# Performance work log

Measured on AMD Instinct MI355X. Metric: run time of the kernel, lower is better.

The kernel has to match this reference:

```python
import jax, jax.numpy as jnp
import numpy as np

N_NODES = 12000
N_EDGES = 384000
F_IN = 128       # num_features
D = 64           # latent_dim (hidden_dim), num_gc_layers = 1
H_DEC = 64       # ceil(F_IN / 2)
BN_EPS = 1e-4


def _gcn_conv(x, W, b, src, dst, n):
    # PyG GCNConv: h = x @ W; add self-loops; sym-normalized scatter-add; + bias
    h = x @ W
    loop = jnp.arange(n)
    s = jnp.concatenate([src, loop])
    d = jnp.concatenate([dst, loop])
    deg = jax.ops.segment_sum(jnp.ones(s.shape[0], dtype=x.dtype), d, num_segments=n)
    dis = jax.lax.rsqrt(deg)  # deg >= 1 thanks to self-loops
    norm = dis[s] * dis[d]    # [E+N]
    out = jax.ops.segment_sum(h[s] * norm[:, None], d, num_segments=n)
    return out + b


def _bn_train(x, gamma, beta):
    # BatchNorm1d, training-mode batch statistics, biased variance, eps=1e-4
    mu = jnp.mean(x, axis=0)
    xc = x - mu
    var = jnp.mean(xc * xc, axis=0)
    return xc * jax.lax.rsqrt(var + BN_EPS) * gamma + beta


def _enc_layer(x, W, b, g, be, src, dst, n):
    # GCNConv -> Sigmoid -> (dropout no-op) -> BatchNorm
    return _bn_train(jax.nn.sigmoid(_gcn_conv(x, W, b, src, dst, n)), g, be)


def setup_inputs() -> dict:
    key = jax.random.key(0)
    ks = jax.random.split(key, 16)
    inp = {
        'x': jax.random.normal(ks[0], (N_NODES, F_IN), dtype=jnp.float32),
        'src': jax.random.randint(ks[1], (N_EDGES,), 0, N_NODES),
        'dst': jax.random.randint(ks[2], (N_EDGES,), 0, N_NODES),
        'batch': jnp.zeros((N_NODES,), dtype=jnp.int32),
        'noise': jax.random.normal(ks[3], (N_NODES, D), dtype=jnp.float32),
        # base_gcn encoder (GCNConv F_IN -> D, BN)
        'W0': jax.random.normal(ks[4], (F_IN, D), dtype=jnp.float32) * 0.08,
        'b0': jnp.zeros((D,), dtype=jnp.float32),
        'g0': jnp.ones((D,), dtype=jnp.float32),
        'be0': jnp.zeros((D,), dtype=jnp.float32),
        # gcn_mean encoder (GCNConv D -> D, BN)
        'Wm': jax.random.normal(ks[5], (D, D), dtype=jnp.float32) * 0.12,
        'bm': jnp.zeros((D,), dtype=jnp.float32),
        'gm': jnp.ones((D,), dtype=jnp.float32),
        'bem': jnp.zeros((D,), dtype=jnp.float32),
        # gcn_logstddev encoder (GCNConv D -> D, BN)
        'Ws': jax.random.normal(ks[6], (D, D), dtype=jnp.float32) * 0.12,
        'bs': jnp.zeros((D,), dtype=jnp.float32),
        'gs': jnp.ones((D,), dtype=jnp.float32),
        'bes': jnp.zeros((D,), dtype=jnp.float32),
        # decoder MLP: Linear(D, H_DEC) -> LeakyReLU -> Linear(H_DEC, F_IN)
        'Dw1': jax.random.normal(ks[7], (D, H_DEC), dtype=jnp.float32) * 0.12,
        'Db1': jnp.zeros((H_DEC,), dtype=jnp.float32),
        'Dw2': jax.random.normal(ks[8], (H_DEC, F_IN), dtype=jnp.float32) * 0.12,
        'Db2': jnp.zeros((F_IN,), dtype=jnp.float32),
    }
    return inp


def reference(x, src, dst, batch, noise,
              W0, b0, g0, be0,
              Wm, bm, gm, bem,
              Ws, bs, gs, bes,
              Dw1, Db1, Dw2, Db2):
    n = x.shape[0]
    hidden = _enc_layer(x, W0, b0, g0, be0, src, dst, n)          # [N, D]
    mean = _enc_layer(hidden, Wm, bm, gm, bem, src, dst, n)       # [N, D]
    logstd = _enc_layer(hidden, Ws, bs, gs, bes, src, dst, n)     # [N, D]
    z = noise * jnp.exp(logstd) + mean                            # reparam trick
    # decoder MLP (LeakyReLU default slope 0.01)
    h = jax.nn.leaky_relu(z @ Dw1 + Db1, negative_slope=0.01)
    reconstructed_x = h @ Dw2 + Db2                               # [N, F_IN]
    A_pred = jax.nn.sigmoid(z @ z.T)                              # [N, N]
    return (reconstructed_x, A_pred)
```

## Files before the change

kernel.cpp:

```cpp
#include <hip/hip_runtime.h>
#include <hip/hip_bf16.h>

#define N_NODES 12000
#define N_EDGES 384000
#define F_INN   128
#define DLAT    64
#define BN_EPS  1e-4f

typedef __attribute__((ext_vector_type(8))) short bf16x8;
typedef __attribute__((ext_vector_type(4))) float f32x4;

__device__ __forceinline__ float sigmoidf(float x) { return 1.0f / (1.0f + __expf(-x)); }

__device__ __forceinline__ unsigned short f2bf_rne(float x) {
    unsigned u = __float_as_uint(x);
    unsigned r = (u + 0x7fffu + ((u >> 16) & 1u)) >> 16;
    return (unsigned short)r;
}
__device__ __forceinline__ float bf2f(unsigned short h) {
    return __uint_as_float((unsigned)h << 16);
}

__global__ void k_init(int* cnt, int* cur, int n) {
    int i = blockIdx.x * blockDim.x + threadIdx.x;
    if (i < n) { cnt[i] = 0; cur[i] = 0; }
}

__global__ void k_count(const int* dst, int* cnt, int e) {
    int i = blockIdx.x * blockDim.x + threadIdx.x;
    if (i < e) atomicAdd(&cnt[dst[i]], 1);
}

__global__ void k_scan(const int* __restrict__ cnt, int* __restrict__ offs,
                       float* __restrict__ dis, int n) {
    __shared__ int wsum[16];
    int tid = threadIdx.x;
    int base = tid * 12;
    int v[12];
    int s = 0;
#pragma unroll
    for (int q = 0; q < 12; q++) {
        int i = base + q;
        v[q] = (i < n) ? cnt[i] : 0;
        s += v[q];
        if (i < n) dis[i] = rsqrtf((float)(v[q] + 1));
    }
    int lane = tid & 63, w = tid >> 6;
    int ps = s;
#pragma unroll
    for (int o = 1; o < 64; o <<= 1) {
        int t2 = __shfl_up(ps, o, 64);
        if (lane >= o) ps += t2;
    }
    if (lane == 63) wsum[w] = ps;
    __syncthreads();
    if (tid == 0) {
        int acc = 0;
        for (int i = 0; i < 16; i++) { int t2 = wsum[i]; wsum[i] = acc; acc += t2; }
    }
    __syncthreads();
    int acc = wsum[w] + ps - s;
#pragma unroll
    for (int q = 0; q < 12; q++) {
        int i = base + q;
        if (i < n) offs[i] = acc;
        acc += v[q];
        if (i == n - 1) offs[n] = acc;
    }
}

__global__ void k_scatter(const int* src, const int* dst, const int* offs, int* cur,
                          int* ssrc, int e) {
    int i = blockIdx.x * blockDim.x + threadIdx.x;
    if (i < e) {
        int d = dst[i];
        int p = atomicAdd(&cur[d], 1);
        ssrc[offs[d] + p] = src[i];
    }
}

__global__ void k_mm(const float* __restrict__ X, int n, int K,
                     const float* __restrict__ Wa, int Ma,
                     const float* __restrict__ Wb, int Mb,
                     float* __restrict__ out) {
    __shared__ float Wl[8192];
    int M = Ma + Mb;
    for (int idx = threadIdx.x; idx < K * M; idx += blockDim.x) {
        int k = idx / M, m = idx % M;
        Wl[idx] = (m < Ma) ? Wa[k * Ma + m] : Wb[k * Mb + (m - Ma)];
    }
    __syncthreads();
    int rpb = blockDim.x / M;
    int r = blockIdx.x * rpb + threadIdx.x / M;
    int m = threadIdx.x % M;
    if (r >= n) return;
    const float* xr = X + (size_t)r * K;
    float acc = 0.f;
    for (int k = 0; k < K; k++) acc += xr[k] * Wl[k * M + m];
    out[(size_t)r * M + m] = acc;
}

__global__ void k_agg(const float* __restrict__ h, const float* __restrict__ dis,
                      const int* __restrict__ offs, const int* __restrict__ ssrc,
                      const float* __restrict__ ba, const float* __restrict__ bb, int Ma,
                      float* __restrict__ out, int dim, int n) {
    int t = blockIdx.x * blockDim.x + threadIdx.x;
    int node = t / dim;
    if (node >= n) return;
    int f = t - node * dim;
    float di = dis[node];
    float acc = h[(size_t)node * dim + f] * di;
    int e0 = offs[node], e1 = offs[node + 1];
    int j = e0;
    for (; j + 3 < e1; j += 4) {
        int s0 = ssrc[j], s1 = ssrc[j + 1], s2 = ssrc[j + 2], s3 = ssrc[j + 3];
        acc += h[(size_t)s0 * dim + f] * dis[s0];
        acc += h[(size_t)s1 * dim + f] * dis[s1];
        acc += h[(size_t)s2 * dim + f] * dis[s2];
        acc += h[(size_t)s3 * dim + f] * dis[s3];
    }
    for (; j < e1; j++) {
        int s = ssrc[j];
        acc += h[(size_t)s * dim + f] * dis[s];
    }
    float bias = (f < Ma) ? ba[f] : bb[f - Ma];
    out[(size_t)node * dim + f] = sigmoidf(acc * di + bias);
}

#define STATS_BLOCKS 64
__global__ void k_stats1(const float* __restrict__ act, int dim, int n,
                         float* __restrict__ part) {
    int rpb = 256 / dim;
    int c = threadIdx.x % dim;
    int rloc = threadIdx.x / dim;
    float s = 0.f, s2 = 0.f;
    for (int r = blockIdx.x * rpb + rloc; r < n; r += STATS_BLOCKS * rpb) {
        float v = act[(size_t)r * dim + c];
        s += v; s2 += v * v;
    }
    __shared__ float sh[512];
    sh[threadIdx.x] = s; sh[256 + threadIdx.x] = s2;
    __syncthreads();
    if (rloc == 0) {
        for (int q = 1; q < rpb; q++) {
            s += sh[q * dim + c];
            s2 += sh[256 + q * dim + c];
        }
        part[(size_t)(blockIdx.x * dim + c) * 2] = s;
        part[(size_t)(blockIdx.x * dim + c) * 2 + 1] = s2;
    }
}

__global__ void k_stats2(const float* __restrict__ part, int dim, int n,
                         float* __restrict__ mu, float* __restrict__ var) {
    int c = threadIdx.x;
    if (c >= dim) return;
    float s = 0.f, s2 = 0.f;
    for (int q = 0; q < STATS_BLOCKS; q++) {
        s += part[(size_t)(q * dim + c) * 2];
        s2 += part[(size_t)(q * dim + c) * 2 + 1];
    }
    float m = s / n;
    mu[c] = m;
    var[c] = s2 / n - m * m;
}

__global__ void k_bnapply(const float* __restrict__ in, float* __restrict__ out,
                          const float* __restrict__ mu, const float* __restrict__ var,
                          const float* __restrict__ g, const float* __restrict__ be,
                          int dim, size_t total) {
    size_t i = (size_t)blockIdx.x * blockDim.x + threadIdx.x;
    if (i >= total) return;
    int f = (int)(i % dim);
    out[i] = (in[i] - mu[f]) * rsqrtf(var[f] + BN_EPS) * g[f] + be[f];
}

__global__ void k_z(const float* __restrict__ act2, const float* __restrict__ noise,
                    const float* __restrict__ mu, const float* __restrict__ var,
                    const float* __restrict__ gm, const float* __restrict__ bem,
                    const float* __restrict__ gs, const float* __restrict__ bes,
                    float* __restrict__ z, unsigned short* __restrict__ zh,
                    unsigned short* __restrict__ zl, int n) {
    int i = blockIdx.x * blockDim.x + threadIdx.x;
    if (i >= 12032 * 64) return;
    int row = i >> 6, j = i & 63;
    if (row >= n) { zh[i] = 0; zl[i] = 0; return; }
    const float* ar = act2 + (size_t)row * 128;
    float m  = (ar[j]      - mu[j])      * rsqrtf(var[j]      + BN_EPS) * gm[j] + bem[j];
    float ls = (ar[j + 64] - mu[j + 64]) * rsqrtf(var[j + 64] + BN_EPS) * gs[j] + bes[j];
    float zv = noise[i] * __expf(ls) + m;
    z[i] = zv;
    unsigned short h = f2bf_rne(zv);
    zh[i] = h;
    zl[i] = f2bf_rne(zv - bf2f(h));
}

__global__ void k_dec(const float* __restrict__ z,
                      const float* __restrict__ W1, const float* __restrict__ B1,
                      const float* __restrict__ W2, const float* __restrict__ B2,
                      float* __restrict__ out, int n) {
    __shared__ float w1[64 * 64];
    __shared__ float w2[64 * 128];
    __shared__ float zl[16 * 64];
    __shared__ float hl[16 * 64];
    int t = threadIdx.x;
    int row0 = blockIdx.x * 16;
    {
        const float4* W14 = (const float4*)W1;
        const float4* W24 = (const float4*)W2;
        for (int i = t; i < 1024; i += 256) ((float4*)w1)[i] = W14[i];
        for (int i = t; i < 2048; i += 256) ((float4*)w2)[i] = W24[i];
        ((float4*)zl)[t] = ((const float4*)(z + (size_t)row0 * 64))[t];
    }
    __syncthreads();
    {
        int hc = t & 63, rg = t >> 6;
        float a0 = B1[hc], a1 = a0, a2 = a0, a3 = a0;
        int rb = rg * 4;
        for (int k = 0; k < 64; k++) {
            float wv = w1[k * 64 + hc];
            a0 += zl[(rb + 0) * 64 + k] * wv;
            a1 += zl[(rb + 1) * 64 + k] * wv;
            a2 += zl[(rb + 2) * 64 + k] * wv;
            a3 += zl[(rb + 3) * 64 + k] * wv;
        }
        hl[(rb + 0) * 64 + hc] = a0 > 0.f ? a0 : 0.01f * a0;
        hl[(rb + 1) * 64 + hc] = a1 > 0.f ? a1 : 0.01f * a1;
        hl[(rb + 2) * 64 + hc] = a2 > 0.f ? a2 : 0.01f * a2;
        hl[(rb + 3) * 64 + hc] = a3 > 0.f ? a3 : 0.01f * a3;
    }
    __syncthreads();
    {
        int oc = t & 127, rg = t >> 7;
        float o[8];
#pragma unroll
        for (int i = 0; i < 8; i++) o[i] = B2[oc];
        int rb = rg * 8;
        for (int k = 0; k < 64; k++) {
            float wv = w2[k * 128 + oc];
#pragma unroll
            for (int i = 0; i < 8; i++) o[i] += hl[(rb + i) * 64 + k] * wv;
        }
#pragma unroll
        for (int i = 0; i < 8; i++)
            out[(size_t)(row0 + rb + i) * 128 + oc] = o[i];
    }
}

#define TN2 94
__global__ __launch_bounds__(256) void k_apred(const unsigned short* __restrict__ zh,
                                               const unsigned short* __restrict__ zl,
                                               float* __restrict__ out, int n) {
    int b = blockIdx.x;
    float ff = (float)(2 * TN2 + 1);
    int bi = (int)((ff - sqrtf(ff * ff - 8.0f * (float)b)) * 0.5f);
    while (bi > 0 && b < bi * TN2 - bi * (bi - 1) / 2) bi--;
    while (b >= (bi + 1) * TN2 - (bi + 1) * bi / 2) bi++;
    int bj = bi + (b - (bi * TN2 - bi * (bi - 1) / 2));
    int i0 = bi * 128, j0 = bj * 128;

    int t = threadIdx.x;
    int wave = t >> 6, lane = t & 63;
    int wr = wave >> 1, wc = wave & 1;
    int lrow = lane & 15;
    int kg   = lane >> 4;

    int arow0 = i0 + wr * 64;
    int brow0 = j0 + wc * 64;

    f32x4 acc[4][4] = {};

#pragma unroll
    for (int kc = 0; kc < 2; kc++) {
        int koff = kc * 32 + kg * 8;
        bf16x8 ah[4], al[4], bh[4], bl[4];
#pragma unroll
        for (int f = 0; f < 4; f++) {
            size_t aoff = (size_t)(arow0 + f * 16 + lrow) * 64 + koff;
            ah[f] = *(const bf16x8*)(zh + aoff);
            al[f] = *(const bf16x8*)(zl + aoff);
            size_t boff = (size_t)(brow0 + f * 16 + lrow) * 64 + koff;
            bh[f] = *(const bf16x8*)(zh + boff);
            bl[f] = *(const bf16x8*)(zl + boff);
        }
#pragma unroll
        for (int fi = 0; fi < 4; fi++)
#pragma unroll
            for (int fj = 0; fj < 4; fj++) {
                acc[fi][fj] = __builtin_amdgcn_mfma_f32_16x16x32_bf16(
                    ah[fi], bh[fj], acc[fi][fj], 0, 0, 0);
                acc[fi][fj] = __builtin_amdgcn_mfma_f32_16x16x32_bf16(
                    ah[fi], bl[fj], acc[fi][fj], 0, 0, 0);
                acc[fi][fj] = __builtin_amdgcn_mfma_f32_16x16x32_bf16(
                    al[fi], bh[fj], acc[fi][fj], 0, 0, 0);
            }
    }

#pragma unroll
    for (int fi = 0; fi < 4; fi++)
#pragma unroll
        for (int fj = 0; fj < 4; fj++)
#pragma unroll
            for (int q = 0; q < 4; q++)
                acc[fi][fj][q] = sigmoidf(acc[fi][fj][q]);

#pragma unroll
    for (int fi = 0; fi < 4; fi++) {
#pragma unroll
        for (int q = 0; q < 4; q++) {
            int r = arow0 + fi * 16 + kg * 4 + q;
            if (r < n) {
#pragma unroll
                for (int fj = 0; fj < 4; fj++) {
                    int c = brow0 + fj * 16 + lrow;
                    if (c < n) out[(size_t)r * n + c] = acc[fi][fj][q];
                }
            }
        }
    }
    if (bi != bj) {
#pragma unroll
        for (int fj = 0; fj < 4; fj++) {
            int c = brow0 + fj * 16 + lrow;
            if (c < n) {
#pragma unroll
                for (int fi = 0; fi < 4; fi++) {
#pragma unroll
                    for (int q = 0; q < 4; q++) {
                        int r = arow0 + fi * 16 + kg * 4 + q;
                        if (r < n) out[(size_t)c * n + r] = acc[fi][fj][q];
                    }
                }
            }
        }
    }
}

extern "C" void kernel_launch(void* const* d_in, const int* in_sizes, int n_in,
                              void* d_out, int out_size, void* d_ws, size_t ws_size,
                              hipStream_t stream) {
    const float* x     = (const float*)d_in[0];
    const int*   src   = (const int*)d_in[1];
    const int*   dst   = (const int*)d_in[2];
    const float* noise = (const float*)d_in[4];
    const float* W0  = (const float*)d_in[5];
    const float* b0  = (const float*)d_in[6];
    const float* g0  = (const float*)d_in[7];
    const float* be0 = (const float*)d_in[8];
    const float* Wm  = (const float*)d_in[9];
    const float* bm  = (const float*)d_in[10];
    const float* gm  = (const float*)d_in[11];
    const float* bem = (const float*)d_in[12];
    const float* Ws  = (const float*)d_in[13];
    const float* bs  = (const float*)d_in[14];
    const float* gs  = (const float*)d_in[15];
    const float* bes = (const float*)d_in[16];
    const float* Dw1 = (const float*)d_in[17];
    const float* Db1 = (const float*)d_in[18];
    const float* Dw2 = (const float*)d_in[19];
    const float* Db2 = (const float*)d_in[20];
    float* out = (float*)d_out;

    const int n = N_NODES, e = N_EDGES;

    int*   cnt  = (int*)d_ws;
    int*   offs = (int*)d_ws + 12032;
    int*   cur  = (int*)d_ws + 24064;
    int*   ssrc = (int*)d_ws + 36096;
    float* dis  = (float*)d_ws + 420096;
    float* mu   = (float*)d_ws + 432128;
    float* var  = (float*)d_ws + 432384;
    float* part = (float*)d_ws + 432640;
    float* bufA = (float*)d_ws + 449024;
    float* bufB = bufA + (size_t)N_NODES * 128;
    float* zbuf = bufB;
    unsigned short* zhbuf = (unsigned short*)((float*)d_ws + 3521024);
    unsigned short* zlbuf = (unsigned short*)((float*)d_ws + 3906048);

    k_init<<<(n + 255) / 256, 256, 0, stream>>>(cnt, cur, n);
    k_count<<<(e + 255) / 256, 256, 0, stream>>>(dst, cnt, e);
    k_scan<<<1, 1024, 0, stream>>>(cnt, offs, dis, n);
    k_scatter<<<(e + 255) / 256, 256, 0, stream>>>(src, dst, offs, cur, ssrc, e);

    k_mm<<<n / 4, 256, 0, stream>>>(x, n, F_INN, W0, DLAT, nullptr, 0, bufA);
    k_agg<<<(n * DLAT) / 256, 256, 0, stream>>>(bufA, dis, offs, ssrc, b0, nullptr, DLAT,
                                                bufB, DLAT, n);
    k_stats1<<<STATS_BLOCKS, 256, 0, stream>>>(bufB, DLAT, n, part);
    k_stats2<<<1, 64, 0, stream>>>(part, DLAT, n, mu, var);
    k_bnapply<<<(n * DLAT) / 256, 256, 0, stream>>>(bufB, bufA, mu, var, g0, be0, DLAT,
                                                    (size_t)n * DLAT);

    k_mm<<<n / 2, 256, 0, stream>>>(bufA, n, DLAT, Wm, DLAT, Ws, DLAT, bufB);
    k_agg<<<(n * 128) / 256, 256, 0, stream>>>(bufB, dis, offs, ssrc, bm, bs, DLAT,
                                               bufA, 128, n);
    k_stats1<<<STATS_BLOCKS, 256, 0, stream>>>(bufA, 128, n, part);
    k_stats2<<<1, 128, 0, stream>>>(part, 128, n, mu, var);

    k_z<<<(12032 * 64) / 256, 256, 0, stream>>>(bufA, noise, mu, var, gm, bem, gs, bes,
                                                zbuf, zhbuf, zlbuf, n);

    k_dec<<<n / 16, 256, 0, stream>>>(zbuf, Dw1, Db1, Dw2, Db2, out, n);

    k_apred<<<TN2 * (TN2 + 1) / 2, 256, 0, stream>>>(zhbuf, zlbuf,
                                                     out + (size_t)n * F_INN, n);
}
```

Before: 1.048 ms.

## Compute full A_pred grid with LDS-staged swizzled tiles instead of symmetric triangle

Replaces the triangular-block launch that wrote each tile and its transpose with a full 2D grid where each block computes only its own 128x128 tile. The z hi/lo tiles are staged into XOR-swizzled shared memory before the MFMA loop, and launch bounds request two blocks per CU. This drops the uncoalesced transposed stores, which dominate the 576 MB output write, at the cost of doubling the MFMA compute and the z reads.

```diff
diff --git a/kernel.cpp b/kernel.cpp
--- a/kernel.cpp
+++ b/kernel.cpp
@@ -248,40 +248,57 @@
 }
 
 #define TN2 94
-__global__ __launch_bounds__(256) void k_apred(const unsigned short* __restrict__ zh,
-                                               const unsigned short* __restrict__ zl,
-                                               float* __restrict__ out, int n) {
-    int b = blockIdx.x;
-    float ff = (float)(2 * TN2 + 1);
-    int bi = (int)((ff - sqrtf(ff * ff - 8.0f * (float)b)) * 0.5f);
-    while (bi > 0 && b < bi * TN2 - bi * (bi - 1) / 2) bi--;
-    while (b >= (bi + 1) * TN2 - (bi + 1) * bi / 2) bi++;
-    int bj = bi + (b - (bi * TN2 - bi * (bi - 1) / 2));
+__global__ __launch_bounds__(256, 2) void k_apred(const unsigned short* __restrict__ zh,
+                                                  const unsigned short* __restrict__ zl,
+                                                  float* __restrict__ out, int n) {
+    __shared__ __align__(16) unsigned short si_h[128 * 64];
+    __shared__ __align__(16) unsigned short si_l[128 * 64];
+    __shared__ __align__(16) unsigned short sj_h[128 * 64];
+    __shared__ __align__(16) unsigned short sj_l[128 * 64];
+
+    int bj = blockIdx.x, bi = blockIdx.y;
     int i0 = bi * 128, j0 = bj * 128;
-
     int t = threadIdx.x;
+
+    auto stage = [&](const unsigned short* __restrict__ g, unsigned short* s, int row0) {
+#pragma unroll
+        for (int q = 0; q < 4; q++) {
+            int u = q * 256 + t;
+            int row = u >> 3, c16 = u & 7;
+            int c16s = c16 ^ (row & 7);
+            *(float4*)((char*)s + row * 128 + c16s * 16) =
+                *(const float4*)(g + (size_t)(row0 + row) * 64 + c16 * 8);
+        }
+    };
+    stage(zh, si_h, i0);
+    stage(zl, si_l, i0);
+    stage(zh, sj_h, j0);
+    stage(zl, sj_l, j0);
+    __syncthreads();
+
     int wave = t >> 6, lane = t & 63;
     int wr = wave >> 1, wc = wave & 1;
     int lrow = lane & 15;
     int kg   = lane >> 4;
 
-    int arow0 = i0 + wr * 64;
-    int brow0 = j0 + wc * 64;
+    auto frag = [&](const unsigned short* s, int tr, int kc) -> bf16x8 {
+        int c16s = (kc * 4 + kg) ^ (tr & 7);
+        return *(const bf16x8*)((const char*)s + tr * 128 + c16s * 16);
+    };
 
     f32x4 acc[4][4] = {};
 
 #pragma unroll
     for (int kc = 0; kc < 2; kc++) {
-        int koff = kc * 32 + kg * 8;
         bf16x8 ah[4], al[4], bh[4], bl[4];
 #pragma unroll
         for (int f = 0; f < 4; f++) {
-            size_t aoff = (size_t)(arow0 + f * 16 + lrow) * 64 + koff;
-            ah[f] = *(const bf16x8*)(zh + aoff);
-            al[f] = *(const bf16x8*)(zl + aoff);
-            size_t boff = (size_t)(brow0 + f * 16 + lrow) * 64 + koff;
-            bh[f] = *(const bf16x8*)(zh + boff);
-            bl[f] = *(const bf16x8*)(zl + boff);
+            int tra = wr * 64 + f * 16 + lrow;
+            ah[f] = frag(si_h, tra, kc);
+            al[f] = frag(si_l, tra, kc);
+            int trb = wc * 64 + f * 16 + lrow;
+            bh[f] = frag(sj_h, trb, kc);
+            bl[f] = frag(sj_l, trb, kc);
         }
 #pragma unroll
         for (int fi = 0; fi < 4; fi++)
@@ -304,32 +321,18 @@
             for (int q = 0; q < 4; q++)
                 acc[fi][fj][q] = sigmoidf(acc[fi][fj][q]);
 
+    int colb = j0 + wc * 64;
 #pragma unroll
     for (int fi = 0; fi < 4; fi++) {
 #pragma unroll
         for (int q = 0; q < 4; q++) {
-            int r = arow0 + fi * 16 + kg * 4 + q;
+            int r = i0 + wr * 64 + fi * 16 + kg * 4 + q;
             if (r < n) {
+                float* orow = out + (size_t)r * n + colb;
 #pragma unroll
                 for (int fj = 0; fj < 4; fj++) {
-                    int c = brow0 + fj * 16 + lrow;
-                    if (c < n) out[(size_t)r * n + c] = acc[fi][fj][q];
-                }
-            }
-        }
-    }
-    if (bi != bj) {
-#pragma unroll
-        for (int fj = 0; fj < 4; fj++) {
-            int c = brow0 + fj * 16 + lrow;
-            if (c < n) {
-#pragma unroll
-                for (int fi = 0; fi < 4; fi++) {
-#pragma unroll
-                    for (int q = 0; q < 4; q++) {
-                        int r = arow0 + fi * 16 + kg * 4 + q;
-                        if (r < n) out[(size_t)c * n + r] = acc[fi][fj][q];
-                    }
+                    int c = fj * 16 + lrow;
+                    if (colb + c < n) orow[c] = acc[fi][fj][q];
                 }
             }
         }
@@ -401,6 +404,8 @@
 
     k_dec<<<n / 16, 256, 0, stream>>>(zbuf, Dw1, Db1, Dw2, Db2, out, n);
 
-    k_apred<<<TN2 * (TN2 + 1) / 2, 256, 0, stream>>>(zhbuf, zlbuf,
-                                                     out + (size_t)n * F_INN, n);
-}
+    {
+        dim3 grid(TN2, TN2);
+        k_apred<<<grid, 256, 0, stream>>>(zhbuf, zlbuf, out + (size_t)n * F_INN, n);
+    }
+}
```

Measured after the change: 952.6 us. 1.1x faster.
